# Kernel optimization log

Measured on AMD Instinct MI355X. Metric: run time of the kernel, lower is better.

Reference implementation:

```python
import jax, jax.numpy as jnp
import numpy as np

HIDDEN = 4096
N_HEAD = 16
HEAD_DIM = HIDDEN // N_HEAD          # 256
ROTARY_DIM = HEAD_DIM // 2           # 128 (partial rotary, GPT-J config)
ROPE_BASE = 10000.0
B, S = 4, 1024


def _apply_rope(x, position_ids):
    # x: [B, S, H, D]; rotate first ROTARY_DIM dims, NeoX/rotate-half style.
    rot, pas = x[..., :ROTARY_DIM], x[..., ROTARY_DIM:]
    inv_freq = 1.0 / (ROPE_BASE ** (jnp.arange(0, ROTARY_DIM, 2, dtype=jnp.float32) / ROTARY_DIM))
    ang = position_ids.astype(jnp.float32)[..., None] * inv_freq      # [B, S, R/2]
    cos = jnp.cos(ang)[:, :, None, :]                                  # [B, S, 1, R/2]
    sin = jnp.sin(ang)[:, :, None, :]
    x1, x2 = rot[..., : ROTARY_DIM // 2], rot[..., ROTARY_DIM // 2:]
    rot_out = jnp.concatenate([x1 * cos - x2 * sin, x2 * cos + x1 * sin], axis=-1)
    return jnp.concatenate([rot_out, pas], axis=-1)


def setup_inputs() -> dict:
    key = jax.random.key(0)
    k1, k2, k3 = jax.random.split(key, 3)
    hidden_states = jax.random.normal(k1, (B, S, HIDDEN), dtype=jnp.float32)
    w_qkv = jax.random.normal(k2, (HIDDEN, 3 * HIDDEN), dtype=jnp.float32) * (HIDDEN ** -0.5)
    w_out = jax.random.normal(k3, (HIDDEN, HIDDEN), dtype=jnp.float32) * (HIDDEN ** -0.5)
    position_ids = jnp.broadcast_to(jnp.arange(S, dtype=jnp.int32)[None, :], (B, S))
    return {"position_ids": position_ids, "hidden_states": hidden_states,
            "w_qkv": w_qkv, "w_out": w_out}


def reference(position_ids, hidden_states, w_qkv, w_out):
    qkv = hidden_states @ w_qkv                       # [B, S, 3H]
    q, k, v = jnp.split(qkv, 3, axis=-1)
    q = q.reshape(B, S, N_HEAD, HEAD_DIM)
    k = k.reshape(B, S, N_HEAD, HEAD_DIM)
    v = v.reshape(B, S, N_HEAD, HEAD_DIM)
    q = _apply_rope(q, position_ids)
    k = _apply_rope(k, position_ids)
    scale = HEAD_DIM ** -0.5
    scores = jnp.einsum('bqhd,bkhd->bhqk', q, k) * scale   # [B, H, S, S]
    causal = jnp.tril(jnp.ones((S, S), dtype=bool))
    scores = jnp.where(causal[None, None], scores, jnp.finfo(scores.dtype).min)
    probs = jax.nn.softmax(scores, axis=-1)
    attn = jnp.einsum('bhqk,bkhd->bqhd', probs, v).reshape(B, S, HIDDEN)
    return attn @ w_out
```

## Files before the change

### kernel.cpp

```cpp
#include <hip/hip_runtime.h>
#include <cstdint>

#define HID  4096
#define NHD  16
#define HDIM 256
#define SEQ  1024
#define BB   4
#define N3   12288
#define TOK  4096

typedef unsigned short u16;
typedef __bf16 bf16x8 __attribute__((ext_vector_type(8)));
typedef float  f32x4  __attribute__((ext_vector_type(4)));
typedef float  f32x16 __attribute__((ext_vector_type(16)));

__device__ __forceinline__ u16 f2b(float f) {
    unsigned u = __builtin_bit_cast(unsigned, f);
    u += 0x7fffu + ((u >> 16) & 1u);
    return (u16)(u >> 16);
}
__device__ __forceinline__ float b2f(u16 v) {
    unsigned u = ((unsigned)v) << 16;
    return __builtin_bit_cast(float, u);
}

typedef __attribute__((address_space(3))) unsigned       lds_u32;
typedef const __attribute__((address_space(1))) unsigned glb_u32;
__device__ __forceinline__ void async16(const void* g, void* l) {
    __builtin_amdgcn_global_load_lds((glb_u32*)g, (lds_u32*)l, 16, 0, 0);
}

__global__ __launch_bounds__(256) void cast_bf16(const float4* __restrict__ in,
                                                 uint4* __restrict__ out, int n8) {
    int i = blockIdx.x * 256 + threadIdx.x;
    if (i >= n8) return;
    float4 a = in[2 * i], b = in[2 * i + 1];
    union { u16 h[8]; uint4 v; } o;
    o.h[0] = f2b(a.x); o.h[1] = f2b(a.y); o.h[2] = f2b(a.z); o.h[3] = f2b(a.w);
    o.h[4] = f2b(b.x); o.h[5] = f2b(b.y); o.h[6] = f2b(b.z); o.h[7] = f2b(b.w);
    out[i] = o.v;
}

__global__ __launch_bounds__(256) void tcast(const float* __restrict__ in,
                                             u16* __restrict__ out, int R, int C) {
    __shared__ u16 sT[64 * 80];
    const int c0 = blockIdx.x * 64, r0 = blockIdx.y * 64;
    const int t = threadIdx.x;
    const int rr = t >> 4, cc = (t & 15) * 4;
    for (int rnd = 0; rnd < 4; rnd++) {
        int r = rnd * 16 + rr;
        float4 v = *(const float4*)(in + (size_t)(r0 + r) * C + c0 + cc);
        sT[(cc + 0) * 80 + r] = f2b(v.x);
        sT[(cc + 1) * 80 + r] = f2b(v.y);
        sT[(cc + 2) * 80 + r] = f2b(v.z);
        sT[(cc + 3) * 80 + r] = f2b(v.w);
    }
    __syncthreads();
    const int orow = t >> 2, oc = (t & 3) * 16;
    u16* dst = out + (size_t)(c0 + orow) * R + r0 + oc;
    *(uint4*)dst       = *(uint4*)&sT[orow * 80 + oc];
    *(uint4*)(dst + 8) = *(uint4*)&sT[orow * 80 + oc + 8];
}

template <bool OUT_BF16>
__global__ __launch_bounds__(512, 2) void gemm256(const u16* __restrict__ A,
                                                  const u16* __restrict__ Bt,
                                                  void* __restrict__ Cout,
                                                  int M, int N, int K) {
    __shared__ alignas(16) u16 lds[65536];
    const int t = threadIdx.x;
    const int lane = t & 63, w = t >> 6;
    const int wm = w >> 2, wn = w & 3;
    const int fm = lane & 15, g = lane >> 4;

    const int nwg = (int)gridDim.x;
    const int cpx = nwg >> 3;
    const int swz = (((int)blockIdx.x) & 7) * cpx + (((int)blockIdx.x) >> 3);
    const int gm = M >> 8;
    const int mblk = swz % gm, nblk = swz / gm;
    const int m0 = mblk << 8, n0 = nblk << 8;

    const int srow = t >> 2;
    const int schk = ((t & 3) ^ (srow & 3) ^ ((srow >> 2) & 2)) * 8;
    const u16* gA = A  + (size_t)(m0 + srow) * K + schk;
    const u16* gB = Bt + (size_t)(n0 + srow) * K + schk;
    const size_t hstep = (size_t)128 * K;
    const int ldst = t * 8;

    const int cxor = (g ^ (fm & 3) ^ ((fm >> 2) & 2)) * 8;
    const int aoff = (wm * 128 + fm) * 32 + cxor;
    const int boff = 16384 + (wn * 64 + fm) * 32 + cxor;

    f32x4 acc[8][4];
#pragma unroll
    for (int i = 0; i < 8; i++)
#pragma unroll
        for (int j = 0; j < 4; j++) acc[i][j] = f32x4{0.f, 0.f, 0.f, 0.f};

    const int nk = K >> 6;

#define STG_A(BO, KT, KS) do { \
    const u16* s_ = gA + (size_t)(KT) * 64 + (KS) * 32; \
    async16(s_,         &lds[(BO) + (KS) * 8192 + ldst]); \
    async16(s_ + hstep, &lds[(BO) + (KS) * 8192 + 4096 + ldst]); } while (0)
#define STG_B(BO, KT, KS) do { \
    const u16* s_ = gB + (size_t)(KT) * 64 + (KS) * 32; \
    async16(s_,         &lds[(BO) + 16384 + (KS) * 8192 + ldst]); \
    async16(s_ + hstep, &lds[(BO) + 16384 + (KS) * 8192 + 4096 + ldst]); } while (0)

    bf16x8 a0[4], a1[4], bfr[4];

#define LD_A0(BO, KS) { _Pragma("unroll") for (int m_ = 0; m_ < 4; m_++) \
    a0[m_] = *(const bf16x8*)&lds[(BO) + (KS) * 8192 + aoff + m_ * 512]; }
#define LD_A1(BO, KS) { _Pragma("unroll") for (int m_ = 0; m_ < 4; m_++) \
    a1[m_] = *(const bf16x8*)&lds[(BO) + (KS) * 8192 + 2048 + aoff + m_ * 512]; }
#define LD_B(BO, KS) { _Pragma("unroll") for (int n_ = 0; n_ < 4; n_++) \
    bfr[n_] = *(const bf16x8*)&lds[(BO) + (KS) * 8192 + boff + n_ * 512]; }
#define MM(AR, MO) { _Pragma("unroll") for (int m_ = 0; m_ < 4; m_++) \
    _Pragma("unroll") for (int n_ = 0; n_ < 4; n_++) \
    acc[(MO) + m_][n_] = __builtin_amdgcn_mfma_f32_16x16x32_bf16(AR[m_], bfr[n_], acc[(MO) + m_][n_], 0, 0, 0); }
#define BARX __builtin_amdgcn_s_barrier()
#define LGKM0 asm volatile("s_waitcnt lgkmcnt(0)" ::: "memory")
#define VM(N_) asm volatile("s_waitcnt vmcnt(" #N_ ")" ::: "memory")
#define PHASE_MID BARX; LGKM0; __builtin_amdgcn_s_setprio(1)
#define PHASE_END __builtin_amdgcn_s_setprio(0); BARX

    STG_A(0, 0, 0); STG_B(0, 0, 0); STG_A(0, 0, 1); STG_B(0, 0, 1);
    VM(4); BARX;

#pragma unroll 1
    for (int kt = 0; kt < nk - 1; kt++) {
        const int bo = (kt & 1) << 15, nb = bo ^ 32768;
        LD_A0(bo, 0); LD_B(bo, 0);
        STG_A(nb, kt + 1, 0);
        PHASE_MID; MM(a0, 0); PHASE_END;
        LD_A1(bo, 0);
        STG_B(nb, kt + 1, 0);
        VM(4);
        PHASE_MID; MM(a1, 4); PHASE_END;
        LD_A0(bo, 1); LD_B(bo, 1);
        STG_A(nb, kt + 1, 1);
        PHASE_MID; MM(a0, 0); PHASE_END;
        LD_A1(bo, 1);
        STG_B(nb, kt + 1, 1);
        VM(4);
        PHASE_MID; MM(a1, 4); PHASE_END;
    }
    {
        const int bo = ((nk - 1) & 1) << 15;
        LD_A0(bo, 0); LD_B(bo, 0);
        PHASE_MID; MM(a0, 0); PHASE_END;
        LD_A1(bo, 0);
        VM(0);
        PHASE_MID; MM(a1, 4); PHASE_END;
        LD_A0(bo, 1); LD_B(bo, 1);
        PHASE_MID; MM(a0, 0); PHASE_END;
        LD_A1(bo, 1);
        PHASE_MID; MM(a1, 4); PHASE_END;
    }

    const int crow0 = m0 + wm * 128 + g * 4;
    const int ccol = n0 + wn * 64 + fm;
#pragma unroll
    for (int mi = 0; mi < 8; mi++)
#pragma unroll
        for (int r = 0; r < 4; r++) {
            const size_t row = (size_t)(crow0 + mi * 16 + r);
            if (OUT_BF16) {
                u16* p = (u16*)Cout + row * N + ccol;
#pragma unroll
                for (int n_ = 0; n_ < 4; n_++) p[n_ * 16] = f2b(acc[mi][n_][r]);
            } else {
                float* p = (float*)Cout + row * N + ccol;
#pragma unroll
                for (int n_ = 0; n_ < 4; n_++) p[n_ * 16] = acc[mi][n_][r];
            }
        }
#undef STG_A
#undef STG_B
#undef LD_A0
#undef LD_A1
#undef LD_B
#undef MM
#undef BARX
#undef LGKM0
#undef VM
#undef PHASE_MID
#undef PHASE_END
}

__global__ __launch_bounds__(256) void rope_tab(const int* __restrict__ pos_ids,
                                                float2* __restrict__ tab) {
    const int idx = blockIdx.x * 256 + threadIdx.x;
    const int bs = idx >> 6, i = idx & 63;
    const float invf = __expf((float)i * -0.14391156831212787f);
    const float ang = (float)pos_ids[bs] * invf;
    float sn, cs;
    __sincosf(ang, &sn, &cs);
    tab[idx] = make_float2(cs, sn);
}

__global__ __launch_bounds__(256) void rope_relayout(const float2* __restrict__ tab,
                                                     const u16* __restrict__ qkv,
                                                     u16* __restrict__ Qo,
                                                     u16* __restrict__ Ko,
                                                     u16* __restrict__ VTo) {
    __shared__ u16 sV[64 * 256];
    const int st = blockIdx.x, h = blockIdx.y, b = blockIdx.z;
    const int t = threadIdx.x;
    const int sbase = st * 64;

    {
        const u16* vbase = qkv + (size_t)(b * SEQ + sbase) * N3 + 2 * HID + h * HDIM;
        const int dcol = (t & 31) * 8;
        const int tokoff = t >> 5;
#pragma unroll
        for (int r = 0; r < 4; r++)
#pragma unroll
            for (int s8 = 0; s8 < 8; s8++) {
                int tok = r * 16 + s8 * 2 + tokoff;
                async16(vbase + (size_t)tok * N3 + dcol, &sV[r * 4096 + s8 * 512 + t * 8]);
            }
    }

    const int tok = t & 63, part = t >> 6;
    const int s = sbase + tok;
    const int isK = part >> 1, isPass = part & 1;
    const u16* src = qkv + (size_t)(b * SEQ + s) * N3 + isK * HID + h * HDIM + isPass * 128;
    u16* dst = (isK ? Ko : Qo) + ((size_t)((b * NHD + h) * SEQ + s)) * HDIM + isPass * 128;
    if (!isPass) {
        const float2* trow = tab + ((size_t)(b * SEQ + s) << 6);
#pragma unroll
        for (int c = 0; c < 8; c++) {
            bf16x8 xa = *(const bf16x8*)(src + c * 8);
            bf16x8 xb = *(const bf16x8*)(src + 64 + c * 8);
            union { u16 h[8]; uint4 v; } o1, o2;
#pragma unroll
            for (int j = 0; j < 8; j++) {
                float2 t2 = trow[c * 8 + j];
                const float cs = t2.x, sn = t2.y;
                float x1 = (float)xa[j], x2 = (float)xb[j];
                o1.h[j] = f2b(x1 * cs - x2 * sn);
                o2.h[j] = f2b(x2 * cs + x1 * sn);
            }
            *(uint4*)(dst + c * 8)      = o1.v;
            *(uint4*)(dst + 64 + c * 8) = o2.v;
        }
    } else {
        const uint4* s4 = (const uint4*)src;
        uint4* d4 = (uint4*)dst;
#pragma unroll
        for (int c = 0; c < 16; c++) d4[c] = s4[c];
    }

    asm volatile("s_waitcnt vmcnt(0)" ::: "memory");
    __syncthreads();

    u16* vt = VTo + ((size_t)((b * NHD + h) * HDIM + t)) * SEQ + sbase;
#pragma unroll
    for (int g = 0; g < 8; g++) {
        union { u16 h[8]; uint4 v; } o;
#pragma unroll
        for (int j = 0; j < 8; j++) o.h[j] = sV[(g * 8 + j) * 256 + t];
        *(uint4*)(vt + g * 8) = o.v;
    }
}

__global__ __launch_bounds__(256) void attn_fwd(const u16* __restrict__ Q,
                                                const u16* __restrict__ K,
                                                const u16* __restrict__ VT,
                                                u16* __restrict__ attnO) {
    __shared__ u16 sK[2][32 * 256];
    __shared__ u16 sVT[2][32 * 256];
    __shared__ u16 sP[4 * 16 * 32];
    const int qt = (int)gridDim.x - 1 - (int)blockIdx.x;
    const int h = blockIdx.y, b = blockIdx.z;
    const int t = threadIdx.x, lane = t & 63, w = t >> 6;
    const int fm = lane & 15, g = lane >> 4, fk = g * 8;
    const int qbase = qt * 64;
    const size_t head = ((size_t)(b * NHD + h)) * SEQ * HDIM;
    const u16* qptr = Q + head + (size_t)(qbase + w * 16 + fm) * HDIM;
    bf16x8 qf[8];
#pragma unroll
    for (int kk = 0; kk < 8; kk++) qf[kk] = *(const bf16x8*)(qptr + kk * 32 + fk);
    const f32x4 z = {0.f, 0.f, 0.f, 0.f};
    f32x4 O[16];
#pragma unroll
    for (int n = 0; n < 16; n++) O[n] = z;
    float mrow[4] = {-1e30f, -1e30f, -1e30f, -1e30f};
    float lrow[4] = {0.f, 0.f, 0.f, 0.f};
    const int nkt = qt * 2 + 2;
    const u16* kbaseP = K + head;
    const u16* vtbase = VT + head;
    const int qg_base = qbase + w * 16 + g * 4;

    const int krow = t >> 5;
    const int dcol = ((t & 31) ^ krow) * 8;
    const int drow = t >> 2;
    const int scol = ((t & 3) ^ (drow & 3)) * 8;

#define STAGE_KV(BUF, KB) do { \
    _Pragma("unroll") for (int r_ = 0; r_ < 4; r_++) \
        async16(kbaseP + (size_t)((KB) * 32 + r_ * 8 + krow) * HDIM + dcol, \
                &sK[BUF][r_ * 2048 + t * 8]); \
    _Pragma("unroll") for (int r_ = 0; r_ < 4; r_++) \
        async16(vtbase + (size_t)(r_ * 64 + drow) * SEQ + (KB) * 32 + scol, \
                &sVT[BUF][r_ * 2048 + t * 8]); } while (0)

    STAGE_KV(0, 0);
    asm volatile("s_waitcnt vmcnt(0)" ::: "memory");
    __syncthreads();

    for (int kb = 0; kb < nkt; kb++) {
        const int cur = kb & 1;
        if (kb + 1 < nkt) STAGE_KV(cur ^ 1, kb + 1);

        f32x4 sc0 = z, sc1 = z;
        __builtin_amdgcn_s_setprio(1);
#pragma unroll
        for (int kk = 0; kk < 8; kk++) {
            const int p = ((kk * 4 + g) ^ (fm & 7)) * 8;
            bf16x8 kf0 = *(const bf16x8*)&sK[cur][fm * 256 + p];
            bf16x8 kf1 = *(const bf16x8*)&sK[cur][(16 + fm) * 256 + p];
            sc0 = __builtin_amdgcn_mfma_f32_16x16x32_bf16(qf[kk], kf0, sc0, 0, 0, 0);
            sc1 = __builtin_amdgcn_mfma_f32_16x16x32_bf16(qf[kk], kf1, sc1, 0, 0, 0);
        }
        __builtin_amdgcn_s_setprio(0);
        const int kg0 = kb * 32 + fm, kg1 = kg0 + 16;
        float alpha[4];
        bool grow = false;
#pragma unroll
        for (int j = 0; j < 4; j++) {
            const int qg = qg_base + j;
            float s0 = (kg0 <= qg) ? sc0[j] * 0.0625f : -1e30f;
            float s1 = (kg1 <= qg) ? sc1[j] * 0.0625f : -1e30f;
            float mx = fmaxf(s0, s1);
            mx = fmaxf(mx, __shfl_xor(mx, 1, 64));
            mx = fmaxf(mx, __shfl_xor(mx, 2, 64));
            mx = fmaxf(mx, __shfl_xor(mx, 4, 64));
            mx = fmaxf(mx, __shfl_xor(mx, 8, 64));
            const float mn = fmaxf(mrow[j], mx);
            grow = grow || (mn > mrow[j]);
            alpha[j] = __expf(mrow[j] - mn);
            mrow[j] = mn;
            float p0 = __expf(s0 - mn);
            float p1 = __expf(s1 - mn);
            float rs = p0 + p1;
            rs += __shfl_xor(rs, 1, 64);
            rs += __shfl_xor(rs, 2, 64);
            rs += __shfl_xor(rs, 4, 64);
            rs += __shfl_xor(rs, 8, 64);
            lrow[j] = lrow[j] * alpha[j] + rs;
            const int r = g * 4 + j;
            sP[w * 512 + r * 32 + fm]      = f2b(p0);
            sP[w * 512 + r * 32 + 16 + fm] = f2b(p1);
        }
        if (__any(grow)) {
#pragma unroll
            for (int n = 0; n < 16; n++) {
                O[n][0] *= alpha[0]; O[n][1] *= alpha[1];
                O[n][2] *= alpha[2]; O[n][3] *= alpha[3];
            }
        }
        bf16x8 pf = *(const bf16x8*)&sP[w * 512 + fm * 32 + fk];
        __builtin_amdgcn_s_setprio(1);
#pragma unroll
        for (int n = 0; n < 16; n++) {
            const int d = n * 16 + fm;
            bf16x8 vf = *(const bf16x8*)&sVT[cur][d * 32 + ((g ^ (fm & 3)) << 3)];
            O[n] = __builtin_amdgcn_mfma_f32_16x16x32_bf16(pf, vf, O[n], 0, 0, 0);
        }
        __builtin_amdgcn_s_setprio(0);
        asm volatile("s_waitcnt vmcnt(0)" ::: "memory");
        __syncthreads();
    }
#undef STAGE_KV
#pragma unroll
    for (int j = 0; j < 4; j++) {
        const int r = g * 4 + j;
        const float inv = 1.0f / lrow[j];
        u16* orow = attnO + (size_t)(b * SEQ + qbase + w * 16 + r) * HID + h * HDIM;
#pragma unroll
        for (int n = 0; n < 16; n++)
            orow[n * 16 + fm] = f2b(O[n][j] * inv);
    }
}

extern "C" void kernel_launch(void* const* d_in, const int* in_sizes, int n_in,
                              void* d_out, int out_size, void* d_ws, size_t ws_size,
                              hipStream_t stream) {
    (void)in_sizes; (void)n_in; (void)out_size; (void)ws_size;
    const int*   pos    = (const int*)d_in[0];
    const float* hidden = (const float*)d_in[1];
    const float* wqkv   = (const float*)d_in[2];
    const float* wout   = (const float*)d_in[3];
    float* out = (float*)d_out;
    char* ws = (char*)d_ws;

    u16* hiddenB = (u16*)ws;
    u16* wqkvT   = (u16*)(ws + (size_t)33554432);
    u16* woutT   = (u16*)(ws + (size_t)134217728);
    u16* qkv     = (u16*)(ws + (size_t)167772160);
    u16* Qb    = wqkvT;
    u16* Kb    = wqkvT + 16777216;
    u16* VTb   = wqkvT + 33554432;
    u16* attnB = qkv;
    float2* tabF = (float2*)ws;

    cast_bf16<<<dim3(TOK * HID / 8 / 256), 256, 0, stream>>>(
        (const float4*)hidden, (uint4*)hiddenB, TOK * HID / 8);
    tcast<<<dim3(N3 / 64, HID / 64), 256, 0, stream>>>(wqkv, wqkvT, HID, N3);
    tcast<<<dim3(HID / 64, HID / 64), 256, 0, stream>>>(wout, woutT, HID, HID);
    gemm256<true><<<dim3((TOK / 256) * (N3 / 256)), 512, 0, stream>>>(
        hiddenB, wqkvT, qkv, TOK, N3, HID);
    rope_tab<<<dim3(BB * SEQ * 64 / 256), 256, 0, stream>>>(pos, tabF);
    rope_relayout<<<dim3(SEQ / 64, NHD, BB), 256, 0, stream>>>(tabF, qkv, Qb, Kb, VTb);
    attn_fwd<<<dim3(SEQ / 64, NHD, BB), 256, 0, stream>>>(Qb, Kb, VTb, attnB);
    gemm256<false><<<dim3((TOK / 256) * (HID / 256)), 512, 0, stream>>>(
        attnB, woutT, out, TOK, HID, HID);
}
```

Baseline: 1.099 ms.

## Rewrite attention with 32x32 MFMA, 128-query tiles, register P via permlane

Reworks the attention kernel to use 32x32x16 bf16 MFMAs with 128-query tiles (32 queries per wave), computing S^T so each lane owns one query row. Probabilities are packed to bf16 and redistributed with permlane32_swap instead of a round trip through shared memory. Fully masked key tiles are skipped per wave, and the grid becomes 1D with a pairing order that mixes heavy and light causal tiles. It also sets launch_bounds occupancy 2. The cost is higher register pressure from 128 accumulator floats plus 16 Q fragments per lane, which may cause spills or lower occupancy.

```diff
diff --git a/kernel.cpp b/kernel.cpp
--- a/kernel.cpp
+++ b/kernel.cpp
@@ -22,6 +22,11 @@
 __device__ __forceinline__ float b2f(u16 v) {
     unsigned u = ((unsigned)v) << 16;
     return __builtin_bit_cast(float, u);
+}
+__device__ __forceinline__ unsigned cvt_pk_bf16(float lo, float hi) {
+    unsigned r;
+    asm("v_cvt_pk_bf16_f32 %0, %1, %2" : "=v"(r) : "v"(lo), "v"(hi));
+    return r;
 }
 
 typedef __attribute__((address_space(3))) unsigned       lds_u32;
@@ -266,46 +271,52 @@
     }
 }
 
-__global__ __launch_bounds__(256) void attn_fwd(const u16* __restrict__ Q,
-                                                const u16* __restrict__ K,
-                                                const u16* __restrict__ VT,
-                                                u16* __restrict__ attnO) {
+__global__ __launch_bounds__(256, 2) void attn_fwd(const u16* __restrict__ Q,
+                                                   const u16* __restrict__ K,
+                                                   const u16* __restrict__ VT,
+                                                   u16* __restrict__ attnO) {
     __shared__ u16 sK[2][32 * 256];
     __shared__ u16 sVT[2][32 * 256];
-    __shared__ u16 sP[4 * 16 * 32];
-    const int qt = (int)gridDim.x - 1 - (int)blockIdx.x;
-    const int h = blockIdx.y, b = blockIdx.z;
+    const int bid = (int)blockIdx.x;
+    const int qt8 = (bid < 256) ? (7 - (bid >> 6)) : ((bid - 256) >> 6);
+    const int bh = bid & 63, h = bh & 15, b = bh >> 4;
     const int t = threadIdx.x, lane = t & 63, w = t >> 6;
-    const int fm = lane & 15, g = lane >> 4, fk = g * 8;
-    const int qbase = qt * 64;
+    const int kid = lane & 31, hh = lane >> 5;
+    const int qb = qt8 * 128;
+    const int qg = qb + w * 32 + kid;
+    const int qmaxw = qb + w * 32 + 31;
     const size_t head = ((size_t)(b * NHD + h)) * SEQ * HDIM;
-    const u16* qptr = Q + head + (size_t)(qbase + w * 16 + fm) * HDIM;
-    bf16x8 qf[8];
-#pragma unroll
-    for (int kk = 0; kk < 8; kk++) qf[kk] = *(const bf16x8*)(qptr + kk * 32 + fk);
-    const f32x4 z = {0.f, 0.f, 0.f, 0.f};
-    f32x4 O[16];
-#pragma unroll
-    for (int n = 0; n < 16; n++) O[n] = z;
-    float mrow[4] = {-1e30f, -1e30f, -1e30f, -1e30f};
-    float lrow[4] = {0.f, 0.f, 0.f, 0.f};
-    const int nkt = qt * 2 + 2;
     const u16* kbaseP = K + head;
     const u16* vtbase = VT + head;
-    const int qg_base = qbase + w * 16 + g * 4;
-
-    const int krow = t >> 5;
-    const int dcol = ((t & 31) ^ krow) * 8;
-    const int drow = t >> 2;
-    const int scol = ((t & 3) ^ (drow & 3)) * 8;
+
+    bf16x8 qf[16];
+    {
+        const u16* qrow = Q + head + (size_t)qg * HDIM + hh * 8;
+#pragma unroll
+        for (int kk = 0; kk < 16; kk++) qf[kk] = *(const bf16x8*)(qrow + kk * 16);
+    }
+
+    f32x16 accO[8];
+#pragma unroll
+    for (int dg = 0; dg < 8; dg++)
+#pragma unroll
+        for (int r = 0; r < 16; r++) accO[dg][r] = 0.f;
+    float mrow = -1e30f, lrow = 0.f;
+
+    const int nkt = qt8 * 4 + 4;
+    const int vsw = (kid >> 3) & 3;
 
 #define STAGE_KV(BUF, KB) do { \
-    _Pragma("unroll") for (int r_ = 0; r_ < 4; r_++) \
-        async16(kbaseP + (size_t)((KB) * 32 + r_ * 8 + krow) * HDIM + dcol, \
-                &sK[BUF][r_ * 2048 + t * 8]); \
-    _Pragma("unroll") for (int r_ = 0; r_ < 4; r_++) \
-        async16(vtbase + (size_t)(r_ * 64 + drow) * SEQ + (KB) * 32 + scol, \
-                &sVT[BUF][r_ * 2048 + t * 8]); } while (0)
+    _Pragma("unroll") for (int r_ = 0; r_ < 4; r_++) { \
+        const int key_ = r_ * 8 + (t >> 5); \
+        const int ck_  = (t & 31) ^ key_; \
+        async16(kbaseP + (size_t)((KB) * 32 + key_) * HDIM + ck_ * 8, \
+                &sK[BUF][r_ * 2048 + t * 8]); } \
+    _Pragma("unroll") for (int r_ = 0; r_ < 4; r_++) { \
+        const int d_ = r_ * 64 + (t >> 2); \
+        const int cv_ = (t & 3) ^ ((d_ >> 3) & 3); \
+        async16(vtbase + (size_t)d_ * SEQ + (KB) * 32 + cv_ * 8, \
+                &sVT[BUF][r_ * 2048 + t * 8]); } } while (0)
 
     STAGE_KV(0, 0);
     asm volatile("s_waitcnt vmcnt(0)" ::: "memory");
@@ -314,76 +325,80 @@
     for (int kb = 0; kb < nkt; kb++) {
         const int cur = kb & 1;
         if (kb + 1 < nkt) STAGE_KV(cur ^ 1, kb + 1);
-
-        f32x4 sc0 = z, sc1 = z;
-        __builtin_amdgcn_s_setprio(1);
-#pragma unroll
-        for (int kk = 0; kk < 8; kk++) {
-            const int p = ((kk * 4 + g) ^ (fm & 7)) * 8;
-            bf16x8 kf0 = *(const bf16x8*)&sK[cur][fm * 256 + p];
-            bf16x8 kf1 = *(const bf16x8*)&sK[cur][(16 + fm) * 256 + p];
-            sc0 = __builtin_amdgcn_mfma_f32_16x16x32_bf16(qf[kk], kf0, sc0, 0, 0, 0);
-            sc1 = __builtin_amdgcn_mfma_f32_16x16x32_bf16(qf[kk], kf1, sc1, 0, 0, 0);
+        if ((kb << 5) <= qmaxw) {
+            f32x16 st;
+#pragma unroll
+            for (int r = 0; r < 16; r++) st[r] = 0.f;
+            __builtin_amdgcn_s_setprio(1);
+#pragma unroll
+            for (int kk = 0; kk < 16; kk++) {
+                bf16x8 kf = *(const bf16x8*)&sK[cur][kid * 256 + ((((kk << 1) + hh) ^ kid) << 3)];
+                st = __builtin_amdgcn_mfma_f32_32x32x16_bf16(kf, qf[kk], st, 0, 0, 0);
+            }
+            __builtin_amdgcn_s_setprio(0);
+            const int kb32 = kb << 5;
+            float p[16];
+            float mt = -1e30f;
+#pragma unroll
+            for (int r = 0; r < 16; r++) {
+                const int kgl = kb32 + (r & 3) + 8 * (r >> 2) + 4 * hh;
+                p[r] = (kgl <= qg) ? st[r] * 0.0625f : -1e30f;
+                mt = fmaxf(mt, p[r]);
+            }
+            mt = fmaxf(mt, __shfl_xor(mt, 32, 64));
+            const float mold = mrow;
+            const float mn = fmaxf(mold, mt);
+            mrow = mn;
+            float rs = 0.f;
+#pragma unroll
+            for (int r = 0; r < 16; r++) { p[r] = __expf(p[r] - mn); rs += p[r]; }
+            rs += __shfl_xor(rs, 32, 64);
+            const float alpha = __expf(mold - mn);
+            lrow = lrow * alpha + rs;
+            if (__any(mn > mold)) {
+#pragma unroll
+                for (int dg = 0; dg < 8; dg++)
+#pragma unroll
+                    for (int r = 0; r < 16; r++) accO[dg][r] *= alpha;
+            }
+            unsigned pw[8];
+#pragma unroll
+            for (int i = 0; i < 8; i++) pw[i] = cvt_pk_bf16(p[2 * i], p[2 * i + 1]);
+            { auto r2 = __builtin_amdgcn_permlane32_swap(pw[0], pw[2], false, false); pw[0] = r2[0]; pw[2] = r2[1]; }
+            { auto r2 = __builtin_amdgcn_permlane32_swap(pw[1], pw[3], false, false); pw[1] = r2[0]; pw[3] = r2[1]; }
+            { auto r2 = __builtin_amdgcn_permlane32_swap(pw[4], pw[6], false, false); pw[4] = r2[0]; pw[6] = r2[1]; }
+            { auto r2 = __builtin_amdgcn_permlane32_swap(pw[5], pw[7], false, false); pw[5] = r2[0]; pw[7] = r2[1]; }
+            union { uint4 q; bf16x8 v; } f0, f1;
+            f0.q = make_uint4(pw[0], pw[1], pw[2], pw[3]);
+            f1.q = make_uint4(pw[4], pw[5], pw[6], pw[7]);
+            __builtin_amdgcn_s_setprio(1);
+#pragma unroll
+            for (int dg = 0; dg < 8; dg++) {
+                bf16x8 vf = *(const bf16x8*)&sVT[cur][(dg * 32 + kid) * 32 + ((hh ^ vsw) << 3)];
+                accO[dg] = __builtin_amdgcn_mfma_f32_32x32x16_bf16(vf, f0.v, accO[dg], 0, 0, 0);
+            }
+#pragma unroll
+            for (int dg = 0; dg < 8; dg++) {
+                bf16x8 vf = *(const bf16x8*)&sVT[cur][(dg * 32 + kid) * 32 + (((2 + hh) ^ vsw) << 3)];
+                accO[dg] = __builtin_amdgcn_mfma_f32_32x32x16_bf16(vf, f1.v, accO[dg], 0, 0, 0);
+            }
+            __builtin_amdgcn_s_setprio(0);
         }
-        __builtin_amdgcn_s_setprio(0);
-        const int kg0 = kb * 32 + fm, kg1 = kg0 + 16;
-        float alpha[4];
-        bool grow = false;
-#pragma unroll
-        for (int j = 0; j < 4; j++) {
-            const int qg = qg_base + j;
-            float s0 = (kg0 <= qg) ? sc0[j] * 0.0625f : -1e30f;
-            float s1 = (kg1 <= qg) ? sc1[j] * 0.0625f : -1e30f;
-            float mx = fmaxf(s0, s1);
-            mx = fmaxf(mx, __shfl_xor(mx, 1, 64));
-            mx = fmaxf(mx, __shfl_xor(mx, 2, 64));
-            mx = fmaxf(mx, __shfl_xor(mx, 4, 64));
-            mx = fmaxf(mx, __shfl_xor(mx, 8, 64));
-            const float mn = fmaxf(mrow[j], mx);
-            grow = grow || (mn > mrow[j]);
-            alpha[j] = __expf(mrow[j] - mn);
-            mrow[j] = mn;
-            float p0 = __expf(s0 - mn);
-            float p1 = __expf(s1 - mn);
-            float rs = p0 + p1;
-            rs += __shfl_xor(rs, 1, 64);
-            rs += __shfl_xor(rs, 2, 64);
-            rs += __shfl_xor(rs, 4, 64);
-            rs += __shfl_xor(rs, 8, 64);
-            lrow[j] = lrow[j] * alpha[j] + rs;
-            const int r = g * 4 + j;
-            sP[w * 512 + r * 32 + fm]      = f2b(p0);
-            sP[w * 512 + r * 32 + 16 + fm] = f2b(p1);
-        }
-        if (__any(grow)) {
-#pragma unroll
-            for (int n = 0; n < 16; n++) {
-                O[n][0] *= alpha[0]; O[n][1] *= alpha[1];
-                O[n][2] *= alpha[2]; O[n][3] *= alpha[3];
-            }
-        }
-        bf16x8 pf = *(const bf16x8*)&sP[w * 512 + fm * 32 + fk];
-        __builtin_amdgcn_s_setprio(1);
-#pragma unroll
-        for (int n = 0; n < 16; n++) {
-            const int d = n * 16 + fm;
-            bf16x8 vf = *(const bf16x8*)&sVT[cur][d * 32 + ((g ^ (fm & 3)) << 3)];
-            O[n] = __builtin_amdgcn_mfma_f32_16x16x32_bf16(pf, vf, O[n], 0, 0, 0);
-        }
-        __builtin_amdgcn_s_setprio(0);
         asm volatile("s_waitcnt vmcnt(0)" ::: "memory");
         __syncthreads();
     }
 #undef STAGE_KV
-#pragma unroll
-    for (int j = 0; j < 4; j++) {
-        const int r = g * 4 + j;
-        const float inv = 1.0f / lrow[j];
-        u16* orow = attnO + (size_t)(b * SEQ + qbase + w * 16 + r) * HID + h * HDIM;
-#pragma unroll
-        for (int n = 0; n < 16; n++)
-            orow[n * 16 + fm] = f2b(O[n][j] * inv);
-    }
+    const float inv = 1.0f / lrow;
+    u16* orow = attnO + (size_t)(b * SEQ + qg) * HID + h * HDIM;
+#pragma unroll
+    for (int dg = 0; dg < 8; dg++)
+#pragma unroll
+        for (int rq = 0; rq < 4; rq++) {
+            union { u16 h4[4]; unsigned long long v; } o;
+#pragma unroll
+            for (int i = 0; i < 4; i++) o.h4[i] = f2b(accO[dg][rq * 4 + i] * inv);
+            *(unsigned long long*)(orow + dg * 32 + rq * 8 + hh * 4) = o.v;
+        }
 }
 
 extern "C" void kernel_launch(void* const* d_in, const int* in_sizes, int n_in,
@@ -415,7 +430,7 @@
         hiddenB, wqkvT, qkv, TOK, N3, HID);
     rope_tab<<<dim3(BB * SEQ * 64 / 256), 256, 0, stream>>>(pos, tabF);
     rope_relayout<<<dim3(SEQ / 64, NHD, BB), 256, 0, stream>>>(tabF, qkv, Qb, Kb, VTb);
-    attn_fwd<<<dim3(SEQ / 64, NHD, BB), 256, 0, stream>>>(Qb, Kb, VTb, attnB);
+    attn_fwd<<<dim3(512), 256, 0, stream>>>(Qb, Kb, VTb, attnB);
     gemm256<false><<<dim3((TOK / 256) * (HID / 256)), 512, 0, stream>>>(
         attnB, woutT, out, TOK, HID, HID);
 }
```

Measured after the change: 1.015 ms. 7.6% less time.
